# Kernel tuning notes

Hardware: AMD Instinct MI355X
Metric: run time of the kernel (lower is better)

The kernel has to match this reference:

```python
import jax, jax.numpy as jnp
import numpy as np

C = 512
B, Q, H, W = 4, 4, 64, 64


def setup_inputs() -> dict:
    key = jax.random.key(0)
    ks = jax.random.split(key, 16)
    s = 1.0 / np.sqrt(C)
    sb = 1.0 / np.sqrt(C // 4)
    return {
        "x1": jax.random.normal(ks[0], (B, C, Q, H, W), jnp.float32),
        "x2": jax.random.normal(ks[1], (B, C, Q, H, W), jnp.float32),
        "Wq": jax.random.normal(ks[2], (C, C), jnp.float32) * s,
        "bq": jnp.zeros((C,), jnp.float32),
        "Wk": jax.random.normal(ks[3], (C, C), jnp.float32) * s,
        "bk": jnp.zeros((C,), jnp.float32),
        "Wv": jax.random.normal(ks[4], (C, C), jnp.float32) * s,
        "bv": jnp.zeros((C,), jnp.float32),
        "Wa1": jax.random.normal(ks[5], (C // 4, C), jnp.float32) * s,
        "ba1": jnp.zeros((C // 4,), jnp.float32),
        "Wa2": jax.random.normal(ks[6], (4, C // 4), jnp.float32) * sb,
        "ba2": jnp.zeros((4,), jnp.float32),
        "Wo": jax.random.normal(ks[7], (C, C), jnp.float32) * s,
        "bo": jnp.zeros((C,), jnp.float32),
        "gamma": jnp.ones((C,), jnp.float32),
        "beta": jnp.zeros((C,), jnp.float32),
    }


def _conv1x1(x, Wt, b):
    # shared 1x1 conv applied independently to each quaternion component
    # x: [B, Cin, Q, H, W] -> [B, Cout, Q, H, W]
    return jnp.einsum("oc,bcqhw->boqhw", Wt, x) + b[None, :, None, None, None]


def reference(x1, x2, Wq, bq, Wk, bk, Wv, bv, Wa1, ba1, Wa2, ba2, Wo, bo, gamma, beta):
    Bn, Cn, Qn, Hn, Wn = x1.shape
    G = Cn // 4  # head dim / channel groups
    q = _conv1x1(x1, Wq, bq)
    k = _conv1x1(x2, Wk, bk)
    v = _conv1x1(x2, Wv, bv)
    # angle gate: C -> C//4 -> relu -> 4, softmax over the 4 gate channels
    aw = jax.nn.softmax(_conv1x1(jax.nn.relu(_conv1x1(x1, Wa1, ba1)), Wa2, ba2), axis=1)  # [B,4,Q,H,W]
    def gate(t):
        return (t.reshape(Bn, G, 4, Qn, Hn, Wn) * aw[:, None]).reshape(Bn, Cn, Qn, Hn, Wn)
    q = gate(q)
    k = gate(k)
    S = Qn * Hn * Wn
    def heads(t):
        # [B,C,Q,H,W] -> [B, 4 heads, G, S]
        return t.reshape(Bn, G, 4, S).transpose(0, 2, 1, 3)
    qh, kh, vh = heads(q), heads(k), heads(v)
    scale = 1.0 / jnp.sqrt(jnp.asarray(G, qh.dtype))
    attn = jax.nn.softmax(jnp.einsum("bhgs,bhfs->bhgf", qh, kh) * scale, axis=-1)  # [B,4,G,G]
    out = jnp.einsum("bhgf,bhfs->bhgs", attn, vh)  # [B,4,G,S]
    out = out.transpose(0, 2, 1, 3).reshape(Bn, Cn, Qn, Hn, Wn)
    out = _conv1x1(out, Wo, bo)
    # IQBN: normalize each (channel, quaternion component) over (B,H,W)
    mean = out.mean(axis=(0, 3, 4), keepdims=True)
    var = out.var(axis=(0, 3, 4), keepdims=True)
    out = (out - mean) / jnp.sqrt(var + 1e-5)
    return out * gamma[None, :, None, None, None] + beta[None, :, None, None, None]
```

## Files before the change

### kernel.cpp

```cpp
#include <hip/hip_runtime.h>


#define DEVI __device__ __forceinline__
typedef unsigned short u16;
typedef __bf16 bf16x8 __attribute__((ext_vector_type(8)));
typedef float f32x4 __attribute__((ext_vector_type(4)));

DEVI float bf2f(unsigned int u) {
  union { unsigned int u; float f; } v; v.u = u << 16; return v.f;
}
DEVI u16 f2bf(float f) {
  union { float f; unsigned int u; } v; v.f = f;
  unsigned int r = v.u + 0x7FFFu + ((v.u >> 16) & 1u);
  return (u16)(r >> 16);
}
DEVI void gload_lds16(const void* gp, void* lp) {
  __builtin_amdgcn_global_load_lds((const __attribute__((address_space(1))) int*)gp,
                                   (__attribute__((address_space(3))) int*)lp, 16, 0, 0);
}

__global__ __launch_bounds__(256) void cvtW_k(const float* __restrict__ Wq, const float* __restrict__ Wk,
                                              const float* __restrict__ Wa1, u16* __restrict__ WQB,
                                              u16* __restrict__ WKB, u16* __restrict__ WA1B) {
  int i = blockIdx.x * 256 + threadIdx.x;
  const float* src; u16* dst; int off;
  if (i < 65536) { src = Wq; dst = WQB; off = i; }
  else if (i < 131072) { src = Wk; dst = WKB; off = i - 65536; }
  else { src = Wa1; dst = WA1B; off = i - 131072; }
  float4 v = reinterpret_cast<const float4*>(src)[off];
  ushort4 o; o.x = f2bf(v.x); o.y = f2bf(v.y); o.z = f2bf(v.z); o.w = f2bf(v.w);
  reinterpret_cast<ushort4*>(dst)[off] = o;
}

__global__ __launch_bounds__(256) void transpose_cvt(const float* __restrict__ in, u16* __restrict__ out,
                                                     int R, int Cc, long sIn, long sOut) {
  __shared__ float tile[64][65];
  const int t = threadIdx.x;
  const int c0 = blockIdx.x * 64, r0 = blockIdx.y * 64, b = blockIdx.z;
  const float* ip = in + (long)b * sIn;
  u16* op = out + (long)b * sOut;
#pragma unroll
  for (int i = 0; i < 4; ++i) {
    int r = (t >> 4) + i * 16;
    int c = (t & 15) * 4;
    float4 v = *reinterpret_cast<const float4*>(ip + (long)(r0 + r) * Cc + c0 + c);
    tile[r][c] = v.x; tile[r][c + 1] = v.y; tile[r][c + 2] = v.z; tile[r][c + 3] = v.w;
  }
  __syncthreads();
#pragma unroll
  for (int i = 0; i < 4; ++i) {
    int c = (t >> 4) + i * 16;
    int r = (t & 15) * 4;
    ushort4 o;
    o.x = f2bf(tile[r][c]); o.y = f2bf(tile[r + 1][c]);
    o.z = f2bf(tile[r + 2][c]); o.w = f2bf(tile[r + 3][c]);
    *reinterpret_cast<ushort4*>(op + (long)(c0 + c) * R + r0 + r) = o;
  }
}

__global__ __launch_bounds__(256) void woh_k(const float* __restrict__ Wo, u16* __restrict__ Woh) {
  int idx = blockIdx.x * 256 + threadIdx.x;
  int h = idx >> 16;
  int o = (idx >> 7) & 511;
  int g = idx & 127;
  union { float f; unsigned int u; } v; v.f = Wo[(long)o * 512 + 4 * g + h];
  unsigned int r = v.u + 0x7FFFu + ((v.u >> 16) & 1u);
  Woh[idx] = (u16)(r >> 16);
}

enum { MODE_GATE = 0, MODE_BIAS = 1, MODE_PLAIN = 2, MODE_FOLD1 = 3 };

template <int MODE>
__global__ __launch_bounds__(256, 2) void gemm_bt(const u16* __restrict__ A, const u16* __restrict__ Bt,
                                                  u16* __restrict__ C, const float* __restrict__ bias,
                                                  const float* __restrict__ aw, float* __restrict__ stata,
                                                  int M, int N, int K, long sA, long sB, long sC) {
  __shared__ u16 As[2][128 * 64];
  __shared__ u16 Bs[2][128 * 64];
  __shared__ float racc[128][2];
  const int t = threadIdx.x;
  const int bn = blockIdx.x, bm = blockIdx.y, bz = blockIdx.z;
  const u16* Ab; const u16* Bb;
  if constexpr (MODE == MODE_FOLD1) {
    Ab = A + (long)(bz & 3) * 512 * 128;
    Bb = Bt + (long)bz * 128 * 128;
  } else {
    Ab = A + (long)bz * sA;
    Bb = Bt + (long)bz * sB;
  }
  const u16* Atile = Ab + (long)(bm * 128) * K;
  const u16* Btile = Bb + (long)(bn * 128) * K;
  const int wid = t >> 6, l = t & 63;
  const int rbase = (wid >> 1) * 64, cbase = (wid & 1) * 64;
  const int lr = l & 15, hi = l >> 4;
  f32x4 acc[4][4] = {};
  const int nt = K >> 6;

#pragma unroll
  for (int i = 0; i < 4; ++i) {
    int idx = t + i * 256;
    int r = idx >> 3;
    int gs = ((idx & 7) ^ (r & 7)) * 8;
    gload_lds16(Atile + (long)r * K + gs, &As[0][idx * 8]);
    gload_lds16(Btile + (long)r * K + gs, &Bs[0][idx * 8]);
  }
  __syncthreads();
  int cur = 0;
  for (int kt = 0; kt < nt; ++kt) {
    if (kt + 1 < nt) {
      int koff = (kt + 1) << 6;
#pragma unroll
      for (int i = 0; i < 4; ++i) {
        int idx = t + i * 256;
        int r = idx >> 3;
        int gs = ((idx & 7) ^ (r & 7)) * 8;
        gload_lds16(Atile + (long)r * K + koff + gs, &As[cur ^ 1][idx * 8]);
        gload_lds16(Btile + (long)r * K + koff + gs, &Bs[cur ^ 1][idx * 8]);
      }
    }
#pragma unroll
    for (int s = 0; s < 2; ++s) {
      bf16x8 av[4], bv[4];
#pragma unroll
      for (int m = 0; m < 4; ++m) {
        int ra = rbase + m * 16 + lr;
        av[m] = *reinterpret_cast<const bf16x8*>(&As[cur][ra * 64 + ((4 * s + hi) ^ (ra & 7)) * 8]);
      }
#pragma unroll
      for (int n = 0; n < 4; ++n) {
        int rb = cbase + n * 16 + lr;
        bv[n] = *reinterpret_cast<const bf16x8*>(&Bs[cur][rb * 64 + ((4 * s + hi) ^ (rb & 7)) * 8]);
      }
#pragma unroll
      for (int m = 0; m < 4; ++m)
#pragma unroll
        for (int n = 0; n < 4; ++n)
          acc[m][n] = __builtin_amdgcn_mfma_f32_16x16x32_bf16(av[m], bv[n], acc[m][n], 0, 0, 0);
    }
    __syncthreads();
    cur ^= 1;
  }

  int qq = 0;
  if constexpr (MODE == MODE_BIAS) {
    if (t < 128) { racc[t][0] = 0.f; racc[t][1] = 0.f; }
    __syncthreads();
    qq = bn >> 5;
  }
#pragma unroll
  for (int m = 0; m < 4; ++m) {
#pragma unroll
    for (int r = 0; r < 4; ++r) {
      int rloc = rbase + m * 16 + hi * 4 + r;
      int row = bm * 128 + rloc;
      float bval = 0.f;
      if constexpr (MODE == MODE_GATE) bval = bias[row];
      if constexpr (MODE == MODE_BIAS) bval = bias[bz * M + row];
      float rs = 0.f, rq = 0.f;
#pragma unroll
      for (int n = 0; n < 4; ++n) {
        int col = bn * 128 + cbase + n * 16 + lr;
        float v = acc[m][n][r] + bval;
        if constexpr (MODE == MODE_GATE) {
          v *= aw[((long)bz * 4 + (row & 3)) * N + col];
          C[((long)(bz * 4 + (row & 3)) * 128 + (row >> 2)) * 16384 + col] = f2bf(v);
        } else if constexpr (MODE == MODE_FOLD1) {
          C[((long)(bz >> 2) * 512 + row) * 512 + 4 * col + (bz & 3)] = f2bf(v);
        } else {
          C[(long)bz * sC + (long)row * N + col] = f2bf(v);
        }
        if constexpr (MODE == MODE_BIAS) { rs += v; rq += v * v; }
      }
      if constexpr (MODE == MODE_BIAS) {
        atomicAdd(&racc[rloc][0], rs);
        atomicAdd(&racc[rloc][1], rq);
      }
    }
  }
  if constexpr (MODE == MODE_BIAS) {
    __syncthreads();
    if (t < 128) {
      int c = bm * 128 + t;
      atomicAdd(&stata[(c * 4 + qq) * 2], racc[t][0]);
      atomicAdd(&stata[(c * 4 + qq) * 2 + 1], racc[t][1]);
    }
  }
}

__global__ __launch_bounds__(256, 2) void gemm_a1_aw(const u16* __restrict__ Wa1b, const u16* __restrict__ X1t,
                                                     const float* __restrict__ ba1, const float* __restrict__ Wa2,
                                                     const float* __restrict__ ba2, float* __restrict__ AW) {
  __shared__ union {
    struct { u16 As[2][128 * 64]; u16 Bs[2][128 * 64]; } st;
    float a1s[128][129];
  } u;
  __shared__ float wa2s[512];
  const int t = threadIdx.x;
  const int bn = blockIdx.x, bz = blockIdx.z;
  for (int i = t; i < 512; i += 256) wa2s[i] = Wa2[i];
  const u16* Btile = X1t + (long)bz * 16384 * 512 + (long)(bn * 128) * 512;
  const int wid = t >> 6, l = t & 63;
  const int rbase = (wid >> 1) * 64, cbase = (wid & 1) * 64;
  const int lr = l & 15, hi = l >> 4;
  f32x4 acc[4][4] = {};
#pragma unroll
  for (int i = 0; i < 4; ++i) {
    int idx = t + i * 256;
    int r = idx >> 3;
    int gs = ((idx & 7) ^ (r & 7)) * 8;
    gload_lds16(Wa1b + (long)r * 512 + gs, &u.st.As[0][idx * 8]);
    gload_lds16(Btile + (long)r * 512 + gs, &u.st.Bs[0][idx * 8]);
  }
  __syncthreads();
  int cur = 0;
  for (int kt = 0; kt < 8; ++kt) {
    if (kt < 7) {
      int koff = (kt + 1) << 6;
#pragma unroll
      for (int i = 0; i < 4; ++i) {
        int idx = t + i * 256;
        int r = idx >> 3;
        int gs = ((idx & 7) ^ (r & 7)) * 8;
        gload_lds16(Wa1b + (long)r * 512 + koff + gs, &u.st.As[cur ^ 1][idx * 8]);
        gload_lds16(Btile + (long)r * 512 + koff + gs, &u.st.Bs[cur ^ 1][idx * 8]);
      }
    }
#pragma unroll
    for (int s = 0; s < 2; ++s) {
      bf16x8 av[4], bv[4];
#pragma unroll
      for (int m = 0; m < 4; ++m) {
        int ra = rbase + m * 16 + lr;
        av[m] = *reinterpret_cast<const bf16x8*>(&u.st.As[cur][ra * 64 + ((4 * s + hi) ^ (ra & 7)) * 8]);
      }
#pragma unroll
      for (int n = 0; n < 4; ++n) {
        int rb = cbase + n * 16 + lr;
        bv[n] = *reinterpret_cast<const bf16x8*>(&u.st.Bs[cur][rb * 64 + ((4 * s + hi) ^ (rb & 7)) * 8]);
      }
#pragma unroll
      for (int m = 0; m < 4; ++m)
#pragma unroll
        for (int n = 0; n < 4; ++n)
          acc[m][n] = __builtin_amdgcn_mfma_f32_16x16x32_bf16(av[m], bv[n], acc[m][n], 0, 0, 0);
    }
    __syncthreads();
    cur ^= 1;
  }
#pragma unroll
  for (int m = 0; m < 4; ++m) {
#pragma unroll
    for (int r = 0; r < 4; ++r) {
      int row = rbase + m * 16 + hi * 4 + r;
      float bval = ba1[row];
#pragma unroll
      for (int n = 0; n < 4; ++n) {
        int col = cbase + n * 16 + lr;
        float v = acc[m][n][r] + bval;
        u.a1s[col][row] = v > 0.f ? v : 0.f;
      }
    }
  }
  __syncthreads();
  if (t < 128) {
    float a0 = ba2[0], a1 = ba2[1], a2 = ba2[2], a3 = ba2[3];
#pragma unroll 4
    for (int c = 0; c < 128; ++c) {
      float av = u.a1s[t][c];
      a0 += wa2s[c] * av; a1 += wa2s[128 + c] * av;
      a2 += wa2s[256 + c] * av; a3 += wa2s[384 + c] * av;
    }
    float mx = fmaxf(fmaxf(a0, a1), fmaxf(a2, a3));
    float e0 = __expf(a0 - mx), e1 = __expf(a1 - mx), e2 = __expf(a2 - mx), e3 = __expf(a3 - mx);
    float inv = 1.f / (e0 + e1 + e2 + e3);
    long sg = (long)bn * 128 + t;
    float* awp = AW + (long)bz * 4 * 16384;
    awp[sg] = e0 * inv;
    awp[16384 + sg] = e1 * inv;
    awp[2 * 16384 + sg] = e2 * inv;
    awp[3 * 16384 + sg] = e3 * inv;
  }
}

__global__ __launch_bounds__(256, 2) void logits_k(const u16* __restrict__ Qh, const u16* __restrict__ Kh,
                                                   float* __restrict__ Lp) {
  __shared__ u16 As[2][128 * 64];
  __shared__ u16 Bs[2][128 * 64];
  const long S = 16384;
  const int ks = blockIdx.x;
  const int bh = blockIdx.y;
  const int t = threadIdx.x;
  const int wid = t >> 6, l = t & 63;
  const int rbase = (wid >> 1) * 64, cbase = (wid & 1) * 64;
  const int lr = l & 15, hi = l >> 4;
  const u16* qb = Qh + (long)bh * 128 * S + ks * 512;
  const u16* kb = Kh + (long)bh * 128 * S + ks * 512;
  f32x4 acc[4][4] = {};
#pragma unroll
  for (int i = 0; i < 4; ++i) {
    int idx = t + i * 256;
    int r = idx >> 3;
    int gs = ((idx & 7) ^ (r & 7)) * 8;
    gload_lds16(qb + (long)r * S + gs, &As[0][idx * 8]);
    gload_lds16(kb + (long)r * S + gs, &Bs[0][idx * 8]);
  }
  __syncthreads();
  int cur = 0;
  for (int kt = 0; kt < 8; ++kt) {
    if (kt < 7) {
      int koff = (kt + 1) << 6;
#pragma unroll
      for (int i = 0; i < 4; ++i) {
        int idx = t + i * 256;
        int r = idx >> 3;
        int gs = ((idx & 7) ^ (r & 7)) * 8;
        gload_lds16(qb + (long)r * S + koff + gs, &As[cur ^ 1][idx * 8]);
        gload_lds16(kb + (long)r * S + koff + gs, &Bs[cur ^ 1][idx * 8]);
      }
    }
#pragma unroll
    for (int s = 0; s < 2; ++s) {
      bf16x8 av[4], bv[4];
#pragma unroll
      for (int m = 0; m < 4; ++m) {
        int ra = rbase + m * 16 + lr;
        av[m] = *reinterpret_cast<const bf16x8*>(&As[cur][ra * 64 + ((4 * s + hi) ^ (ra & 7)) * 8]);
      }
#pragma unroll
      for (int n = 0; n < 4; ++n) {
        int rb = cbase + n * 16 + lr;
        bv[n] = *reinterpret_cast<const bf16x8*>(&Bs[cur][rb * 64 + ((4 * s + hi) ^ (rb & 7)) * 8]);
      }
#pragma unroll
      for (int m = 0; m < 4; ++m)
#pragma unroll
        for (int n = 0; n < 4; ++n)
          acc[m][n] = __builtin_amdgcn_mfma_f32_16x16x32_bf16(av[m], bv[n], acc[m][n], 0, 0, 0);
    }
    __syncthreads();
    cur ^= 1;
  }
  float* Lb = Lp + ((long)ks * 16 + bh) * 16384;
#pragma unroll
  for (int m = 0; m < 4; ++m)
#pragma unroll
    for (int r = 0; r < 4; ++r) {
      int row = rbase + m * 16 + hi * 4 + r;
#pragma unroll
      for (int n = 0; n < 4; ++n) {
        int col = cbase + n * 16 + lr;
        Lb[row * 128 + col] = acc[m][n][r];
      }
    }
}

__global__ __launch_bounds__(256) void softmax_attnT(const float* __restrict__ Lp, u16* __restrict__ attnT) {
  const float scale = 0.08838834764831845f;
  int row = blockIdx.x * 4 + (threadIdx.x >> 6);
  int l = threadIdx.x & 63;
  int bh = row >> 7, g = row & 127;
  const float* base = Lp + (long)bh * 16384 + (long)g * 128;
  float v0 = 0.f, v1 = 0.f;
#pragma unroll 4
  for (int sp = 0; sp < 32; ++sp) {
    v0 += base[(long)sp * 16 * 16384 + l];
    v1 += base[(long)sp * 16 * 16384 + l + 64];
  }
  v0 *= scale; v1 *= scale;
  float m = fmaxf(v0, v1);
  for (int off = 32; off; off >>= 1) m = fmaxf(m, __shfl_xor(m, off));
  float e0 = __expf(v0 - m), e1 = __expf(v1 - m);
  float s = e0 + e1;
  for (int off = 32; off; off >>= 1) s += __shfl_xor(s, off);
  float inv = 1.f / s;
  u16* at = attnT + (long)bh * 16384 + g;
  at[(long)l * 128] = f2bf(e0 * inv);
  at[(long)(l + 64) * 128] = f2bf(e1 * inv);
}

__global__ __launch_bounds__(256) void b2_k(const u16* __restrict__ Weff, const float* __restrict__ bv,
                                            const float* __restrict__ bo, float* __restrict__ b2) {
  int idx = blockIdx.x * 256 + threadIdx.x;
  int b = idx >> 9, o = idx & 511;
  const u16* w = Weff + ((long)b * 512 + o) * 512;
  float s = bo[o];
  for (int c = 0; c < 512; ++c) s += bf2f(w[c]) * bv[c];
  b2[idx] = s;
}

__global__ __launch_bounds__(256) void norm_k(const u16* __restrict__ o2, const float* __restrict__ stata,
                                              const float* __restrict__ gamma, const float* __restrict__ beta,
                                              float* __restrict__ out) {
  long i8 = ((long)blockIdx.x * 256 + threadIdx.x) * 8;
  int c = (int)((i8 >> 14) & 511);
  int s = (int)(i8 & 16383);
  int g0 = c * 4 + (s >> 12);
  float sum = stata[g0 * 2], sq = stata[g0 * 2 + 1];
  float mean = sum * (1.f / 16384.f);
  float var = sq * (1.f / 16384.f) - mean * mean;
  float inv = rsqrtf(var + 1e-5f);
  float sc = inv * gamma[c];
  float sh = beta[c] - mean * sc;
  uint4 v = *reinterpret_cast<const uint4*>(o2 + i8);
  const unsigned int* pv = reinterpret_cast<const unsigned int*>(&v);
  float4 ra, rb;
  ra.x = bf2f(pv[0] & 0xffffu) * sc + sh; ra.y = bf2f(pv[0] >> 16) * sc + sh;
  ra.z = bf2f(pv[1] & 0xffffu) * sc + sh; ra.w = bf2f(pv[1] >> 16) * sc + sh;
  rb.x = bf2f(pv[2] & 0xffffu) * sc + sh; rb.y = bf2f(pv[2] >> 16) * sc + sh;
  rb.z = bf2f(pv[3] & 0xffffu) * sc + sh; rb.w = bf2f(pv[3] >> 16) * sc + sh;
  *reinterpret_cast<float4*>(out + i8) = ra;
  *reinterpret_cast<float4*>(out + i8 + 4) = rb;
}

extern "C" void kernel_launch(void* const* d_in, const int* in_sizes, int n_in,
                              void* d_out, int out_size, void* d_ws, size_t ws_size,
                              hipStream_t stream) {
  const float* x1 = (const float*)d_in[0];
  const float* x2 = (const float*)d_in[1];
  const float* Wq = (const float*)d_in[2];
  const float* bq = (const float*)d_in[3];
  const float* Wk = (const float*)d_in[4];
  const float* bk = (const float*)d_in[5];
  const float* Wv = (const float*)d_in[6];
  const float* bv = (const float*)d_in[7];
  const float* Wa1 = (const float*)d_in[8];
  const float* ba1 = (const float*)d_in[9];
  const float* Wa2 = (const float*)d_in[10];
  const float* ba2 = (const float*)d_in[11];
  const float* Wo = (const float*)d_in[12];
  const float* bo = (const float*)d_in[13];
  const float* gamma = (const float*)d_in[14];
  const float* beta = (const float*)d_in[15];
  float* out = (float*)d_out;

  char* ws = (char*)d_ws;
  const long MB = 1024L * 1024L;
  u16* X1T = (u16*)(ws);
  u16* X2T = (u16*)(ws + 64 * MB);
  u16* Qh  = (u16*)(ws + 128 * MB);
  u16* Kh  = (u16*)(ws + 192 * MB);
  float* AW = (float*)(ws + 256 * MB);
  float* STATA = (float*)(ws + 257 * MB);
  u16* ATT  = (u16*)(ws + 258 * MB);
  u16* WEFF = (u16*)(ws + 259 * MB);
  u16* W2   = (u16*)(ws + 261 * MB);
  u16* WQB  = (u16*)(ws + 263 * MB);
  u16* WKB  = (u16*)(ws + 263 * MB + 512 * 1024);
  u16* WA1B = (u16*)(ws + 264 * MB);
  u16* WVT  = (u16*)(ws + 264 * MB + 256 * 1024);
  u16* WOH  = (u16*)(ws + 264 * MB + 768 * 1024);
  float* B2 = (float*)(ws + 265 * MB + 256 * 1024);
  float* Lp = (float*)(ws);
  u16* O2 = X1T;
  (void)ws_size; (void)in_sizes; (void)n_in; (void)out_size;

  dim3 blk(256);
  const long SC = (long)16384 * 512;

  cvtW_k<<<dim3(576), blk, 0, stream>>>(Wq, Wk, Wa1, WQB, WKB, WA1B);
  woh_k<<<dim3(1024), blk, 0, stream>>>(Wo, WOH);
  transpose_cvt<<<dim3(8, 8, 1), blk, 0, stream>>>(Wv, WVT, 512, 512, 0, 0);
  transpose_cvt<<<dim3(256, 8, 4), blk, 0, stream>>>(x1, X1T, 512, 16384, SC, SC);
  transpose_cvt<<<dim3(256, 8, 4), blk, 0, stream>>>(x2, X2T, 512, 16384, SC, SC);
  hipMemsetAsync(STATA, 0, 2048 * 2 * sizeof(float), stream);

  gemm_a1_aw<<<dim3(128, 1, 4), blk, 0, stream>>>(WA1B, X1T, ba1, Wa2, ba2, AW);

  gemm_bt<MODE_GATE><<<dim3(128, 4, 4), blk, 0, stream>>>(WQB, X1T, Qh, bq, AW, nullptr,
                                                          512, 16384, 512, 0L, SC, SC);
  gemm_bt<MODE_GATE><<<dim3(128, 4, 4), blk, 0, stream>>>(WKB, X2T, Kh, bk, AW, nullptr,
                                                          512, 16384, 512, 0L, SC, SC);

  logits_k<<<dim3(32, 16), blk, 0, stream>>>(Qh, Kh, Lp);
  softmax_attnT<<<dim3(512), blk, 0, stream>>>(Lp, ATT);

  gemm_bt<MODE_FOLD1><<<dim3(1, 4, 16), blk, 0, stream>>>(WOH, ATT, WEFF, nullptr, nullptr, nullptr,
                                                          512, 128, 128, 0L, 0L, 0L);
  b2_k<<<dim3(8), blk, 0, stream>>>(WEFF, bv, bo, B2);
  gemm_bt<MODE_PLAIN><<<dim3(4, 4, 4), blk, 0, stream>>>(WEFF, WVT, W2, nullptr, nullptr, nullptr,
                                                         512, 512, 512, 512L * 512L, 0L, 512L * 512L);

  gemm_bt<MODE_BIAS><<<dim3(128, 4, 4), blk, 0, stream>>>(W2, X2T, O2, B2, nullptr, STATA,
                                                          512, 16384, 512, 512L * 512L, SC, SC);

  norm_k<<<dim3(16384), blk, 0, stream>>>(O2, STATA, gamma, beta, out);
}
```

Baseline: 762.1 us.

## Replace double-buffered LDS pipelines with single-buffer load-sync-compute loops in GEMM kernels

The three MFMA GEMM kernels (gemm_bt, gemm_a1_aw, logits_k) drop their two-stage LDS double buffer and instead load each 64-wide K tile, synchronize, compute, then synchronize again. LDS use per block roughly halves, and the racc scratch now shares storage with the tiles through a union, so more blocks can be resident per CU. The launch-bounds minimum-occupancy hint of 2 is removed. In exchange, global-to-LDS loads no longer overlap MFMA work within a block, so the kernels depend on other resident blocks to hide memory latency.

```diff
diff --git a/kernel.cpp b/kernel.cpp
--- a/kernel.cpp
+++ b/kernel.cpp
@@ -71,13 +71,14 @@
 enum { MODE_GATE = 0, MODE_BIAS = 1, MODE_PLAIN = 2, MODE_FOLD1 = 3 };
 
 template <int MODE>
-__global__ __launch_bounds__(256, 2) void gemm_bt(const u16* __restrict__ A, const u16* __restrict__ Bt,
-                                                  u16* __restrict__ C, const float* __restrict__ bias,
-                                                  const float* __restrict__ aw, float* __restrict__ stata,
-                                                  int M, int N, int K, long sA, long sB, long sC) {
-  __shared__ u16 As[2][128 * 64];
-  __shared__ u16 Bs[2][128 * 64];
-  __shared__ float racc[128][2];
+__global__ __launch_bounds__(256) void gemm_bt(const u16* __restrict__ A, const u16* __restrict__ Bt,
+                                               u16* __restrict__ C, const float* __restrict__ bias,
+                                               const float* __restrict__ aw, float* __restrict__ stata,
+                                               int M, int N, int K, long sA, long sB, long sC) {
+  __shared__ union {
+    struct { u16 As[128 * 64]; u16 Bs[128 * 64]; } st;
+    float racc[128][2];
+  } sm;
   const int t = threadIdx.x;
   const int bn = blockIdx.x, bm = blockIdx.y, bz = blockIdx.z;
   const u16* Ab; const u16* Bb;
@@ -94,42 +95,28 @@
   const int rbase = (wid >> 1) * 64, cbase = (wid & 1) * 64;
   const int lr = l & 15, hi = l >> 4;
   f32x4 acc[4][4] = {};
-  const int nt = K >> 6;
-
-#pragma unroll
-  for (int i = 0; i < 4; ++i) {
-    int idx = t + i * 256;
-    int r = idx >> 3;
-    int gs = ((idx & 7) ^ (r & 7)) * 8;
-    gload_lds16(Atile + (long)r * K + gs, &As[0][idx * 8]);
-    gload_lds16(Btile + (long)r * K + gs, &Bs[0][idx * 8]);
-  }
-  __syncthreads();
-  int cur = 0;
-  for (int kt = 0; kt < nt; ++kt) {
-    if (kt + 1 < nt) {
-      int koff = (kt + 1) << 6;
-#pragma unroll
-      for (int i = 0; i < 4; ++i) {
-        int idx = t + i * 256;
-        int r = idx >> 3;
-        int gs = ((idx & 7) ^ (r & 7)) * 8;
-        gload_lds16(Atile + (long)r * K + koff + gs, &As[cur ^ 1][idx * 8]);
-        gload_lds16(Btile + (long)r * K + koff + gs, &Bs[cur ^ 1][idx * 8]);
-      }
-    }
+  for (int kt = 0; kt < K; kt += 64) {
+#pragma unroll
+    for (int i = 0; i < 4; ++i) {
+      int idx = t + i * 256;
+      int r = idx >> 3;
+      int gs = ((idx & 7) ^ (r & 7)) * 8;
+      gload_lds16(Atile + (long)r * K + kt + gs, &sm.st.As[idx * 8]);
+      gload_lds16(Btile + (long)r * K + kt + gs, &sm.st.Bs[idx * 8]);
+    }
+    __syncthreads();
 #pragma unroll
     for (int s = 0; s < 2; ++s) {
       bf16x8 av[4], bv[4];
 #pragma unroll
       for (int m = 0; m < 4; ++m) {
         int ra = rbase + m * 16 + lr;
-        av[m] = *reinterpret_cast<const bf16x8*>(&As[cur][ra * 64 + ((4 * s + hi) ^ (ra & 7)) * 8]);
+        av[m] = *reinterpret_cast<const bf16x8*>(&sm.st.As[ra * 64 + ((4 * s + hi) ^ (ra & 7)) * 8]);
       }
 #pragma unroll
       for (int n = 0; n < 4; ++n) {
         int rb = cbase + n * 16 + lr;
-        bv[n] = *reinterpret_cast<const bf16x8*>(&Bs[cur][rb * 64 + ((4 * s + hi) ^ (rb & 7)) * 8]);
+        bv[n] = *reinterpret_cast<const bf16x8*>(&sm.st.Bs[rb * 64 + ((4 * s + hi) ^ (rb & 7)) * 8]);
       }
 #pragma unroll
       for (int m = 0; m < 4; ++m)
@@ -138,12 +125,11 @@
           acc[m][n] = __builtin_amdgcn_mfma_f32_16x16x32_bf16(av[m], bv[n], acc[m][n], 0, 0, 0);
     }
     __syncthreads();
-    cur ^= 1;
   }
 
   int qq = 0;
   if constexpr (MODE == MODE_BIAS) {
-    if (t < 128) { racc[t][0] = 0.f; racc[t][1] = 0.f; }
+    if (t < 128) { sm.racc[t][0] = 0.f; sm.racc[t][1] = 0.f; }
     __syncthreads();
     qq = bn >> 5;
   }
@@ -172,8 +158,8 @@
         if constexpr (MODE == MODE_BIAS) { rs += v; rq += v * v; }
       }
       if constexpr (MODE == MODE_BIAS) {
-        atomicAdd(&racc[rloc][0], rs);
-        atomicAdd(&racc[rloc][1], rq);
+        atomicAdd(&sm.racc[rloc][0], rs);
+        atomicAdd(&sm.racc[rloc][1], rq);
       }
     }
   }
@@ -181,17 +167,17 @@
     __syncthreads();
     if (t < 128) {
       int c = bm * 128 + t;
-      atomicAdd(&stata[(c * 4 + qq) * 2], racc[t][0]);
-      atomicAdd(&stata[(c * 4 + qq) * 2 + 1], racc[t][1]);
-    }
-  }
-}
-
-__global__ __launch_bounds__(256, 2) void gemm_a1_aw(const u16* __restrict__ Wa1b, const u16* __restrict__ X1t,
-                                                     const float* __restrict__ ba1, const float* __restrict__ Wa2,
-                                                     const float* __restrict__ ba2, float* __restrict__ AW) {
+      atomicAdd(&stata[(c * 4 + qq) * 2], sm.racc[t][0]);
+      atomicAdd(&stata[(c * 4 + qq) * 2 + 1], sm.racc[t][1]);
+    }
+  }
+}
+
+__global__ __launch_bounds__(256) void gemm_a1_aw(const u16* __restrict__ Wa1b, const u16* __restrict__ X1t,
+                                                  const float* __restrict__ ba1, const float* __restrict__ Wa2,
+                                                  const float* __restrict__ ba2, float* __restrict__ AW) {
   __shared__ union {
-    struct { u16 As[2][128 * 64]; u16 Bs[2][128 * 64]; } st;
+    struct { u16 As[128 * 64]; u16 Bs[128 * 64]; } st;
     float a1s[128][129];
   } u;
   __shared__ float wa2s[512];
@@ -203,40 +189,28 @@
   const int rbase = (wid >> 1) * 64, cbase = (wid & 1) * 64;
   const int lr = l & 15, hi = l >> 4;
   f32x4 acc[4][4] = {};
-#pragma unroll
-  for (int i = 0; i < 4; ++i) {
-    int idx = t + i * 256;
-    int r = idx >> 3;
-    int gs = ((idx & 7) ^ (r & 7)) * 8;
-    gload_lds16(Wa1b + (long)r * 512 + gs, &u.st.As[0][idx * 8]);
-    gload_lds16(Btile + (long)r * 512 + gs, &u.st.Bs[0][idx * 8]);
-  }
-  __syncthreads();
-  int cur = 0;
-  for (int kt = 0; kt < 8; ++kt) {
-    if (kt < 7) {
-      int koff = (kt + 1) << 6;
-#pragma unroll
-      for (int i = 0; i < 4; ++i) {
-        int idx = t + i * 256;
-        int r = idx >> 3;
-        int gs = ((idx & 7) ^ (r & 7)) * 8;
-        gload_lds16(Wa1b + (long)r * 512 + koff + gs, &u.st.As[cur ^ 1][idx * 8]);
-        gload_lds16(Btile + (long)r * 512 + koff + gs, &u.st.Bs[cur ^ 1][idx * 8]);
-      }
-    }
+  for (int kt = 0; kt < 512; kt += 64) {
+#pragma unroll
+    for (int i = 0; i < 4; ++i) {
+      int idx = t + i * 256;
+      int r = idx >> 3;
+      int gs = ((idx & 7) ^ (r & 7)) * 8;
+      gload_lds16(Wa1b + (long)r * 512 + kt + gs, &u.st.As[idx * 8]);
+      gload_lds16(Btile + (long)r * 512 + kt + gs, &u.st.Bs[idx * 8]);
+    }
+    __syncthreads();
 #pragma unroll
     for (int s = 0; s < 2; ++s) {
       bf16x8 av[4], bv[4];
 #pragma unroll
       for (int m = 0; m < 4; ++m) {
         int ra = rbase + m * 16 + lr;
-        av[m] = *reinterpret_cast<const bf16x8*>(&u.st.As[cur][ra * 64 + ((4 * s + hi) ^ (ra & 7)) * 8]);
+        av[m] = *reinterpret_cast<const bf16x8*>(&u.st.As[ra * 64 + ((4 * s + hi) ^ (ra & 7)) * 8]);
       }
 #pragma unroll
       for (int n = 0; n < 4; ++n) {
         int rb = cbase + n * 16 + lr;
-        bv[n] = *reinterpret_cast<const bf16x8*>(&u.st.Bs[cur][rb * 64 + ((4 * s + hi) ^ (rb & 7)) * 8]);
+        bv[n] = *reinterpret_cast<const bf16x8*>(&u.st.Bs[rb * 64 + ((4 * s + hi) ^ (rb & 7)) * 8]);
       }
 #pragma unroll
       for (int m = 0; m < 4; ++m)
@@ -245,7 +219,6 @@
           acc[m][n] = __builtin_amdgcn_mfma_f32_16x16x32_bf16(av[m], bv[n], acc[m][n], 0, 0, 0);
     }
     __syncthreads();
-    cur ^= 1;
   }
 #pragma unroll
   for (int m = 0; m < 4; ++m) {
@@ -282,10 +255,10 @@
   }
 }
 
-__global__ __launch_bounds__(256, 2) void logits_k(const u16* __restrict__ Qh, const u16* __restrict__ Kh,
-                                                   float* __restrict__ Lp) {
-  __shared__ u16 As[2][128 * 64];
-  __shared__ u16 Bs[2][128 * 64];
+__global__ __launch_bounds__(256) void logits_k(const u16* __restrict__ Qh, const u16* __restrict__ Kh,
+                                                float* __restrict__ Lp) {
+  __shared__ u16 As[128 * 64];
+  __shared__ u16 Bs[128 * 64];
   const long S = 16384;
   const int ks = blockIdx.x;
   const int bh = blockIdx.y;
@@ -296,40 +269,28 @@
   const u16* qb = Qh + (long)bh * 128 * S + ks * 512;
   const u16* kb = Kh + (long)bh * 128 * S + ks * 512;
   f32x4 acc[4][4] = {};
-#pragma unroll
-  for (int i = 0; i < 4; ++i) {
-    int idx = t + i * 256;
-    int r = idx >> 3;
-    int gs = ((idx & 7) ^ (r & 7)) * 8;
-    gload_lds16(qb + (long)r * S + gs, &As[0][idx * 8]);
-    gload_lds16(kb + (long)r * S + gs, &Bs[0][idx * 8]);
-  }
-  __syncthreads();
-  int cur = 0;
-  for (int kt = 0; kt < 8; ++kt) {
-    if (kt < 7) {
-      int koff = (kt + 1) << 6;
-#pragma unroll
-      for (int i = 0; i < 4; ++i) {
-        int idx = t + i * 256;
-        int r = idx >> 3;
-        int gs = ((idx & 7) ^ (r & 7)) * 8;
-        gload_lds16(qb + (long)r * S + koff + gs, &As[cur ^ 1][idx * 8]);
-        gload_lds16(kb + (long)r * S + koff + gs, &Bs[cur ^ 1][idx * 8]);
-      }
-    }
+  for (int kt = 0; kt < 512; kt += 64) {
+#pragma unroll
+    for (int i = 0; i < 4; ++i) {
+      int idx = t + i * 256;
+      int r = idx >> 3;
+      int gs = ((idx & 7) ^ (r & 7)) * 8;
+      gload_lds16(qb + (long)r * S + kt + gs, &As[idx * 8]);
+      gload_lds16(kb + (long)r * S + kt + gs, &Bs[idx * 8]);
+    }
+    __syncthreads();
 #pragma unroll
     for (int s = 0; s < 2; ++s) {
       bf16x8 av[4], bv[4];
 #pragma unroll
       for (int m = 0; m < 4; ++m) {
         int ra = rbase + m * 16 + lr;
-        av[m] = *reinterpret_cast<const bf16x8*>(&As[cur][ra * 64 + ((4 * s + hi) ^ (ra & 7)) * 8]);
+        av[m] = *reinterpret_cast<const bf16x8*>(&As[ra * 64 + ((4 * s + hi) ^ (ra & 7)) * 8]);
       }
 #pragma unroll
       for (int n = 0; n < 4; ++n) {
         int rb = cbase + n * 16 + lr;
-        bv[n] = *reinterpret_cast<const bf16x8*>(&Bs[cur][rb * 64 + ((4 * s + hi) ^ (rb & 7)) * 8]);
+        bv[n] = *reinterpret_cast<const bf16x8*>(&Bs[rb * 64 + ((4 * s + hi) ^ (rb & 7)) * 8]);
       }
 #pragma unroll
       for (int m = 0; m < 4; ++m)
@@ -338,7 +299,6 @@
           acc[m][n] = __builtin_amdgcn_mfma_f32_16x16x32_bf16(av[m], bv[n], acc[m][n], 0, 0, 0);
     }
     __syncthreads();
-    cur ^= 1;
   }
   float* Lb = Lp + ((long)ks * 16 + bh) * 16384;
 #pragma unroll
```

Result: slower. 847.5 us (+11.2%).
